# Optimization experiments

Hardware: AMD Instinct MI355X
Metric: run time of the kernel (lower is better)

The kernel has to match this reference:

```python
import jax, jax.numpy as jnp
import numpy as np
import math

D_MODEL = 1024
N_HEADS = 16
B, T = 4, 2048


def setup_inputs() -> dict:
    key = jax.random.key(0)
    ks = jax.random.split(key, 10)
    s = 1.0 / math.sqrt(D_MODEL)
    x = jax.random.normal(ks[0], (B, T, D_MODEL), dtype=jnp.float32)
    # causal mask, broadcastable over batch and heads; 0 -> masked
    mask = jnp.tril(jnp.ones((T, T), dtype=jnp.int32))[None, None, :, :]
    w_q = jax.random.normal(ks[1], (D_MODEL, D_MODEL), dtype=jnp.float32) * s
    b_q = jnp.zeros((D_MODEL,), dtype=jnp.float32)
    w_k = jax.random.normal(ks[2], (D_MODEL, D_MODEL), dtype=jnp.float32) * s
    b_k = jnp.zeros((D_MODEL,), dtype=jnp.float32)
    w_v = jax.random.normal(ks[3], (D_MODEL, D_MODEL), dtype=jnp.float32) * s
    b_v = jnp.zeros((D_MODEL,), dtype=jnp.float32)
    w_o = jax.random.normal(ks[4], (D_MODEL, D_MODEL), dtype=jnp.float32) * s
    b_o = jnp.zeros((D_MODEL,), dtype=jnp.float32)
    return {"x": x, "mask": mask, "w_q": w_q, "b_q": b_q, "w_k": w_k,
            "b_k": b_k, "w_v": w_v, "b_v": b_v, "w_o": w_o, "b_o": b_o}


def reference(x, mask, w_q, b_q, w_k, b_k, w_v, b_v, w_o, b_o):
    Bx, Tx, C = x.shape
    H = N_HEADS
    d_k = C // H
    def split_heads(y):  # [B,T,C] -> [B,H,T,d_k]
        return y.reshape(Bx, Tx, H, d_k).transpose(0, 2, 1, 3)
    Q = split_heads(x @ w_q + b_q)
    K = split_heads(x @ w_k + b_k)
    V = split_heads(x @ w_v + b_v)
    scores = jnp.einsum('bhqd,bhkd->bhqk', Q, K) / math.sqrt(d_k)
    scores = jnp.where(mask == 0, jnp.float32(-1e9), scores)
    attn = jax.nn.softmax(scores, axis=-1)
    out = jnp.einsum('bhqk,bhkd->bhqd', attn, V)
    out = out.transpose(0, 2, 1, 3).reshape(Bx, Tx, C)
    return out @ w_o + b_o
```

## Files before the change

### kernel.cpp

```cpp
#include <hip/hip_runtime.h>
#include <stdint.h>

#define D_MODEL 1024
#define NH      16
#define BB      4
#define TT      2048
#define MROWS   (BB * TT)

typedef __attribute__((ext_vector_type(8))) short bf16x8;
typedef __attribute__((ext_vector_type(4))) float f32x4;

__device__ __forceinline__ unsigned short f2bf(float f) {
    union { float f; unsigned int u; } v; v.f = f;
    unsigned int r = v.u + 0x7fffu + ((v.u >> 16) & 1u);
    return (unsigned short)(r >> 16);
}

__device__ __forceinline__ unsigned short f2bf_fast(float f) {
    union { float f; unsigned int u; } v; v.f = f;
    return (unsigned short)((v.u + 0x8000u) >> 16);
}

__device__ __forceinline__ void gload_lds16(const unsigned short* g, unsigned short* l) {
    __builtin_amdgcn_global_load_lds(
        (const __attribute__((address_space(1))) void*)g,
        (__attribute__((address_space(3))) void*)l,
        16, 0, 0);
}

__global__ void convert_x_kernel(const float* __restrict__ x, unsigned short* __restrict__ xb) {
    int i = blockIdx.x * 256 + threadIdx.x;
    float4 v = ((const float4*)x)[i];
    ushort4 o;
    o.x = f2bf(v.x); o.y = f2bf(v.y); o.z = f2bf(v.z); o.w = f2bf(v.w);
    ((ushort4*)xb)[i] = o;
}

__global__ void transpose_w_kernel(const float* __restrict__ wq, const float* __restrict__ wk,
                                   const float* __restrict__ wv, const float* __restrict__ wo,
                                   unsigned short* tq, unsigned short* tk,
                                   unsigned short* tv, unsigned short* to_) {
    const float* src; unsigned short* dst;
    switch (blockIdx.z) {
        case 0:  src = wq; dst = tq; break;
        case 1:  src = wk; dst = tk; break;
        case 2:  src = wv; dst = tv; break;
        default: src = wo; dst = to_; break;
    }
    __shared__ float tile[32][33];
    int tx = threadIdx.x & 31, ty = threadIdx.x >> 5;
    int k0 = blockIdx.y * 32, n0 = blockIdx.x * 32;
    #pragma unroll
    for (int i = 0; i < 4; ++i)
        tile[ty + i * 8][tx] = src[(k0 + ty + i * 8) * D_MODEL + n0 + tx];
    __syncthreads();
    #pragma unroll
    for (int i = 0; i < 4; ++i)
        dst[(n0 + ty + i * 8) * D_MODEL + k0 + tx] = f2bf(tile[tx][ty + i * 8]);
}

__device__ __forceinline__ void gemm_mainloop(const unsigned short* __restrict__ A,
                                              const unsigned short* __restrict__ Bt,
                                              int m0, int n0,
                                              unsigned short* As, unsigned short* Bs,
                                              f32x4 acc[4][4]) {
    const int tid = threadIdx.x;
    const int lane = tid & 63, wave = tid >> 6;
    const int wm = (wave >> 1) * 64, wn = (wave & 1) * 64;
    const int l15 = lane & 15, quad = lane >> 4;
    const int rx7 = l15 & 7;
    const int srow = tid >> 3;
    const int scol = ((tid & 7) ^ (srow & 7)) * 8;
    const unsigned short* Ag = A + (size_t)(m0 + srow) * D_MODEL + scol;
    const unsigned short* Bg = Bt + (size_t)(n0 + srow) * D_MODEL + scol;
    unsigned short* AsW = As + wave * 512;
    unsigned short* BsW = Bs + wave * 512;
    for (int k0 = 0; k0 < D_MODEL; k0 += 64) {
        __syncthreads();
        #pragma unroll
        for (int p = 0; p < 4; ++p) {
            gload_lds16(Ag + k0 + (size_t)(32 * p) * D_MODEL, AsW + (32 * p) * 64);
            gload_lds16(Bg + k0 + (size_t)(32 * p) * D_MODEL, BsW + (32 * p) * 64);
        }
        __syncthreads();
        #pragma unroll
        for (int kk = 0; kk < 2; ++kk) {
            const int co = ((kk * 4 + quad) ^ rx7) * 8;
            bf16x8 af[4], bfr[4];
            #pragma unroll
            for (int mt = 0; mt < 4; ++mt)
                af[mt] = *(const bf16x8*)(As + (wm + mt * 16 + l15) * 64 + co);
            #pragma unroll
            for (int nt = 0; nt < 4; ++nt)
                bfr[nt] = *(const bf16x8*)(Bs + (wn + nt * 16 + l15) * 64 + co);
            #pragma unroll
            for (int mt = 0; mt < 4; ++mt)
                #pragma unroll
                for (int nt = 0; nt < 4; ++nt)
                    acc[mt][nt] = __builtin_amdgcn_mfma_f32_16x16x32_bf16(af[mt], bfr[nt], acc[mt][nt], 0, 0, 0);
        }
    }
}

__global__ __launch_bounds__(256, 2) void gemm_qkv_kernel(
        const unsigned short* __restrict__ Xb, const unsigned short* __restrict__ Wt,
        const float* __restrict__ bq, const float* __restrict__ bk, const float* __restrict__ bv,
        unsigned short* __restrict__ Qo, unsigned short* __restrict__ Ko,
        unsigned short* __restrict__ VTo) {
    __shared__ unsigned short S[18432];
    unsigned short* As = S;
    unsigned short* Bs = S + 8192;
    int m0 = blockIdx.y * 128, n0 = blockIdx.x * 128;
    f32x4 acc[4][4];
    #pragma unroll
    for (int mt = 0; mt < 4; ++mt)
        #pragma unroll
        for (int nt = 0; nt < 4; ++nt)
            acc[mt][nt] = (f32x4){0.f, 0.f, 0.f, 0.f};
    gemm_mainloop(Xb, Wt, m0, n0, As, Bs, acc);

    const int sel = n0 >> 10;
    const float* bias = (sel == 0) ? bq : (sel == 1) ? bk : bv;
    const float scale = (sel == 0) ? 0.125f * 1.44269504f : 1.f;
    const int tid = threadIdx.x, lane = tid & 63, wave = tid >> 6;
    const int wm = (wave >> 1) * 64, wn = (wave & 1) * 64, l15 = lane & 15, quad = lane >> 4;
    if (sel < 2) {
        unsigned short* Out = (sel == 0) ? Qo : Ko;
        __syncthreads();
        unsigned short* R = S + (wn >> 6) * 9216;
        #pragma unroll
        for (int nt = 0; nt < 4; ++nt) {
            int ln = nt * 16 + l15;
            int col = (n0 + wn + nt * 16 + l15) & 1023;
            float bv_ = bias[col];
            #pragma unroll
            for (int mt = 0; mt < 4; ++mt)
                #pragma unroll
                for (int r = 0; r < 4; ++r) {
                    int lm = wm + mt * 16 + quad * 4 + r;
                    R[lm * 72 + ln] = f2bf((acc[mt][nt][r] + bv_) * scale);
                }
        }
        __syncthreads();
        int hh = tid >> 7, t = tid & 127;
        int h0 = (n0 & 1023) >> 6;
        int b = m0 >> 11, tb = m0 & 2047;
        unsigned short* gp = Out + (size_t)((b * NH + h0 + hh) * TT + tb + t) * 64;
        const unsigned short* lp = S + hh * 9216 + t * 72;
        #pragma unroll
        for (int j = 0; j < 8; ++j)
            *(uint4*)(gp + j * 8) = *(const uint4*)(lp + j * 8);
    } else {
        #pragma unroll
        for (int nt = 0; nt < 4; ++nt) {
            int col = (n0 + wn + nt * 16 + l15) & 1023;
            float bv_ = bias[col];
            int h = col >> 6, dd = col & 63;
            #pragma unroll
            for (int mt = 0; mt < 4; ++mt) {
                int gm0 = m0 + wm + mt * 16 + quad * 4;
                int b = gm0 >> 11, t0 = gm0 & 2047;
                ushort4 o;
                o.x = f2bf(acc[mt][nt][0] + bv_);
                o.y = f2bf(acc[mt][nt][1] + bv_);
                o.z = f2bf(acc[mt][nt][2] + bv_);
                o.w = f2bf(acc[mt][nt][3] + bv_);
                *(ushort4*)&VTo[(((size_t)(b * NH + h) * 16 + (t0 >> 7)) * 64 + dd) * 128 + (t0 & 127)] = o;
            }
        }
    }
}

__global__ __launch_bounds__(256, 2) void gemm_out_kernel(
        const unsigned short* __restrict__ Ob, const unsigned short* __restrict__ Wto,
        const float* __restrict__ bo, float* __restrict__ out) {
    __shared__ unsigned short As[128 * 64], Bs[128 * 64];
    int m0 = blockIdx.y * 128, n0 = blockIdx.x * 128;
    f32x4 acc[4][4];
    #pragma unroll
    for (int mt = 0; mt < 4; ++mt)
        #pragma unroll
        for (int nt = 0; nt < 4; ++nt)
            acc[mt][nt] = (f32x4){0.f, 0.f, 0.f, 0.f};
    gemm_mainloop(Ob, Wto, m0, n0, As, Bs, acc);
    const int tid = threadIdx.x, lane = tid & 63, wave = tid >> 6;
    const int wm = (wave >> 1) * 64, wn = (wave & 1) * 64, l15 = lane & 15, quad = lane >> 4;
    #pragma unroll
    for (int nt = 0; nt < 4; ++nt) {
        int gn = n0 + wn + nt * 16 + l15;
        float bv_ = bo[gn];
        #pragma unroll
        for (int mt = 0; mt < 4; ++mt) {
            #pragma unroll
            for (int r = 0; r < 4; ++r) {
                int gm = m0 + wm + mt * 16 + quad * 4 + r;
                out[(size_t)gm * D_MODEL + gn] = acc[mt][nt][r] + bv_;
            }
        }
    }
}

__global__ __launch_bounds__(256, 3) void flash_kernel(
        const unsigned short* __restrict__ Q, const unsigned short* __restrict__ K,
        const unsigned short* __restrict__ VT, unsigned short* __restrict__ O) {
    __shared__ unsigned short S[21504];
    unsigned short* Kd = S;
    unsigned short* Vd = S + 8192;
    unsigned short* Ps = S + 16384;
    const int n = blockIdx.x;
    const int bh = n & 63;
    const int qt = 15 - (n >> 6);
    const int q0 = qt * 128;
    const int tid = threadIdx.x, lane = tid & 63, wave = tid >> 6;
    const int l15 = lane & 15, quad = lane >> 4;
    const int mbase = wave * 32;
    const unsigned short* Qb = Q + (size_t)bh * (TT * 64) + (size_t)q0 * 64;
    const unsigned short* Kb = K + (size_t)bh * (TT * 64);
    const unsigned short* Vtb = VT + (size_t)bh * (16 * 8192);
    unsigned short* Pw = Ps + wave * 1280;

    int koff[2], voff[2];
    #pragma unroll
    for (int p = 0; p < 2; ++p) {
        int c = p * 256 + tid;
        int r = c >> 3, s = c & 7;
        koff[p] = r * 64 + ((s ^ (r & 7)) * 8);
        voff[p] = r * 128 + ((s ^ (r & 7)) * 8);
    }
    auto fire = [&](int kt, int buf) {
        const unsigned short* Ksrc = Kb + kt * 4096;
        const unsigned short* Vsrc = Vtb + (kt >> 1) * 8192 + (kt & 1) * 64;
        #pragma unroll
        for (int p = 0; p < 2; ++p) {
            gload_lds16(Ksrc + koff[p], Kd + buf * 4096 + (p * 256 + wave * 64) * 8);
            gload_lds16(Vsrc + voff[p], Vd + buf * 4096 + (p * 256 + wave * 64) * 8);
        }
    };

    bf16x8 qf[2][2];
    #pragma unroll
    for (int mt = 0; mt < 2; ++mt)
        #pragma unroll
        for (int kk = 0; kk < 2; ++kk)
            qf[mt][kk] = *(const bf16x8*)(Qb + (size_t)(mbase + mt * 16 + l15) * 64 + kk * 32 + quad * 8);

    float l_part[2][4];
    f32x4 acc[2][4];
    #pragma unroll
    for (int mt = 0; mt < 2; ++mt) {
        #pragma unroll
        for (int r = 0; r < 4; ++r) l_part[mt][r] = 0.f;
        #pragma unroll
        for (int nt = 0; nt < 4; ++nt) acc[mt][nt] = (f32x4){0.f, 0.f, 0.f, 0.f};
    }

    fire(0, 0);

    const int nkt = 2 * qt + 2;
    for (int kt = 0; kt < nkt; ++kt) {
        const int p = kt & 1;
        __syncthreads();
        if (kt + 1 < nkt) fire(kt + 1, p ^ 1);
        if (kt * 64 > q0 + mbase + 31) continue;
        const unsigned short* Ksl = Kd + p * 4096;
        const unsigned short* Vsl = Vd + p * 4096;

        #pragma unroll 1
        for (int s4 = 0; s4 < 2; ++s4) {
            f32x4 sf[2][2];
            #pragma unroll
            for (int mt = 0; mt < 2; ++mt)
                #pragma unroll
                for (int ntl = 0; ntl < 2; ++ntl) sf[mt][ntl] = (f32x4){0.f, 0.f, 0.f, 0.f};
            __builtin_amdgcn_s_setprio(1);
            #pragma unroll
            for (int kk = 0; kk < 2; ++kk)
                #pragma unroll
                for (int ntl = 0; ntl < 2; ++ntl) {
                    int row = s4 * 32 + ntl * 16 + l15;
                    bf16x8 kf = *(const bf16x8*)&Ksl[row * 64 + (((kk * 4 + quad) ^ (row & 7)) * 8)];
                    #pragma unroll
                    for (int mt = 0; mt < 2; ++mt)
                        sf[mt][ntl] = __builtin_amdgcn_mfma_f32_16x16x32_bf16(qf[mt][kk], kf, sf[mt][ntl], 0, 0, 0);
                }
            __builtin_amdgcn_s_setprio(0);
            if (kt >= 2 * qt) {
                const int kofs = (kt - 2 * qt) * 64;
                #pragma unroll
                for (int mt = 0; mt < 2; ++mt)
                    #pragma unroll
                    for (int ntl = 0; ntl < 2; ++ntl)
                        #pragma unroll
                        for (int r = 0; r < 4; ++r) {
                            int qi = mbase + mt * 16 + quad * 4 + r;
                            int ki = kofs + s4 * 32 + ntl * 16 + l15;
                            if (ki > qi) sf[mt][ntl][r] = -1e30f;
                        }
            }
            #pragma unroll
            for (int mt = 0; mt < 2; ++mt)
                #pragma unroll
                for (int ntl = 0; ntl < 2; ++ntl)
                    #pragma unroll
                    for (int r = 0; r < 4; ++r) {
                        float pv = __builtin_amdgcn_exp2f(sf[mt][ntl][r]);
                        l_part[mt][r] += pv;
                        Pw[(mt * 16 + quad * 4 + r) * 40 + ntl * 16 + l15] = f2bf_fast(pv);
                    }
            bf16x8 pa[2];
            #pragma unroll
            for (int mt = 0; mt < 2; ++mt)
                pa[mt] = *(const bf16x8*)&Pw[(mt * 16 + l15) * 40 + quad * 8];
            __builtin_amdgcn_s_setprio(1);
            #pragma unroll
            for (int ntv = 0; ntv < 4; ++ntv) {
                int d = ntv * 16 + l15;
                bf16x8 vf = *(const bf16x8*)&Vsl[d * 64 + (((s4 * 4 + quad) ^ (d & 7)) * 8)];
                #pragma unroll
                for (int mt = 0; mt < 2; ++mt)
                    acc[mt][ntv] = __builtin_amdgcn_mfma_f32_16x16x32_bf16(pa[mt], vf, acc[mt][ntv], 0, 0, 0);
            }
            __builtin_amdgcn_s_setprio(0);
        }
    }

    const int b = bh >> 4, h = bh & 15;
    float inv[2][4];
    #pragma unroll
    for (int mt = 0; mt < 2; ++mt)
        #pragma unroll
        for (int r = 0; r < 4; ++r) {
            float l = l_part[mt][r];
            l += __shfl_xor(l, 1); l += __shfl_xor(l, 2);
            l += __shfl_xor(l, 4); l += __shfl_xor(l, 8);
            inv[mt][r] = __builtin_amdgcn_rcpf(l);
        }
    __syncthreads();
    unsigned short* Ost = S;
    #pragma unroll
    for (int mt = 0; mt < 2; ++mt)
        #pragma unroll
        for (int nt = 0; nt < 4; ++nt)
            #pragma unroll
            for (int r = 0; r < 4; ++r)
                Ost[(mbase + mt * 16 + quad * 4 + r) * 72 + nt * 16 + l15] =
                    f2bf(acc[mt][nt][r] * inv[mt][r]);
    __syncthreads();
    {
        int row = tid >> 1, seg = tid & 1;
        unsigned short* gp = O + (size_t)(b * TT + q0 + row) * D_MODEL + h * 64 + seg * 32;
        const unsigned short* lp = Ost + row * 72 + seg * 32;
        #pragma unroll
        for (int j = 0; j < 4; ++j)
            *(uint4*)(gp + j * 8) = *(const uint4*)(lp + j * 8);
    }
}

extern "C" void kernel_launch(void* const* d_in, const int* in_sizes, int n_in,
                              void* d_out, int out_size, void* d_ws, size_t ws_size,
                              hipStream_t stream) {
    const float* x  = (const float*)d_in[0];
    const float* wq = (const float*)d_in[2];
    const float* bq = (const float*)d_in[3];
    const float* wk = (const float*)d_in[4];
    const float* bk = (const float*)d_in[5];
    const float* wv = (const float*)d_in[6];
    const float* bv = (const float*)d_in[7];
    const float* wo = (const float*)d_in[8];
    const float* bo = (const float*)d_in[9];

    char* ws = (char*)d_ws;
    unsigned short* Xb  = (unsigned short*)ws;
    unsigned short* Wtq = (unsigned short*)(ws + (size_t)(16 << 20));
    unsigned short* Wtk = Wtq + (size_t)D_MODEL * D_MODEL;
    unsigned short* Wtv = Wtk + (size_t)D_MODEL * D_MODEL;
    unsigned short* Wto = Wtv + (size_t)D_MODEL * D_MODEL;
    unsigned short* Qb  = Wto + (size_t)D_MODEL * D_MODEL;
    unsigned short* Kb  = Qb + (size_t)MROWS * D_MODEL;
    unsigned short* VTb = Kb + (size_t)MROWS * D_MODEL;
    unsigned short* Ob  = Xb;

    convert_x_kernel<<<(MROWS * D_MODEL) / (256 * 4), 256, 0, stream>>>(x, Xb);
    transpose_w_kernel<<<dim3(32, 32, 4), 256, 0, stream>>>(wq, wk, wv, wo, Wtq, Wtk, Wtv, Wto);
    gemm_qkv_kernel<<<dim3(3 * D_MODEL / 128, MROWS / 128), 256, 0, stream>>>(
        Xb, Wtq, bq, bk, bv, Qb, Kb, VTb);
    flash_kernel<<<dim3(16 * 64), 256, 0, stream>>>(Qb, Kb, VTb, Ob);
    gemm_out_kernel<<<dim3(D_MODEL / 128, MROWS / 128), 256, 0, stream>>>(Ob, Wto, bo, (float*)d_out);
}
```

Measured before the change: 263.9 us.

## Keep softmax P in registers via transposed QK^T and 16x16x16 MFMA

Swaps the MFMA operands for QK^T so each lane holds scores for one query row across four key columns. That layout matches the A-operand of a 16x16x16 bf16 MFMA, so P is packed straight into registers and the LDS round-trip for P is gone. The PV product now uses 16x16x16 MFMAs with 4-element V loads, and the row-sum reduction is reorganized with cross-quad shuffles. Shared memory shrinks, so launch bounds rise to 4 blocks per CU. The tradeoff is twice as many smaller MFMA instructions and narrower LDS reads for V.

After: 264.4 us. No clear change (+0.2%).

```diff
diff --git a/kernel.cpp b/kernel.cpp
--- a/kernel.cpp
+++ b/kernel.cpp
@@ -8,6 +8,7 @@
 #define MROWS   (BB * TT)
 
 typedef __attribute__((ext_vector_type(8))) short bf16x8;
+typedef __attribute__((ext_vector_type(4))) short bf16x4;
 typedef __attribute__((ext_vector_type(4))) float f32x4;
 
 __device__ __forceinline__ unsigned short f2bf(float f) {
@@ -19,6 +20,11 @@
 __device__ __forceinline__ unsigned short f2bf_fast(float f) {
     union { float f; unsigned int u; } v; v.f = f;
     return (unsigned short)((v.u + 0x8000u) >> 16);
+}
+
+__device__ __forceinline__ f32x4 mfma_16x16x16_bf16(bf16x4 a, bf16x4 b, f32x4 c) {
+    asm("v_mfma_f32_16x16x16_bf16 %0, %1, %2, %0" : "+v"(c) : "v"(a), "v"(b));
+    return c;
 }
 
 __device__ __forceinline__ void gload_lds16(const unsigned short* g, unsigned short* l) {
@@ -200,13 +206,12 @@
     }
 }
 
-__global__ __launch_bounds__(256, 3) void flash_kernel(
+__global__ __launch_bounds__(256, 4) void flash_kernel(
         const unsigned short* __restrict__ Q, const unsigned short* __restrict__ K,
         const unsigned short* __restrict__ VT, unsigned short* __restrict__ O) {
-    __shared__ unsigned short S[21504];
+    __shared__ unsigned short S[16384];
     unsigned short* Kd = S;
     unsigned short* Vd = S + 8192;
-    unsigned short* Ps = S + 16384;
     const int n = blockIdx.x;
     const int bh = n & 63;
     const int qt = 15 - (n >> 6);
@@ -217,7 +222,6 @@
     const unsigned short* Qb = Q + (size_t)bh * (TT * 64) + (size_t)q0 * 64;
     const unsigned short* Kb = K + (size_t)bh * (TT * 64);
     const unsigned short* Vtb = VT + (size_t)bh * (16 * 8192);
-    unsigned short* Pw = Ps + wave * 1280;
 
     int koff[2], voff[2];
     #pragma unroll
@@ -244,15 +248,12 @@
         for (int kk = 0; kk < 2; ++kk)
             qf[mt][kk] = *(const bf16x8*)(Qb + (size_t)(mbase + mt * 16 + l15) * 64 + kk * 32 + quad * 8);
 
-    float l_part[2][4];
+    float l_full[2] = {0.f, 0.f};
     f32x4 acc[2][4];
     #pragma unroll
-    for (int mt = 0; mt < 2; ++mt) {
-        #pragma unroll
-        for (int r = 0; r < 4; ++r) l_part[mt][r] = 0.f;
+    for (int mt = 0; mt < 2; ++mt)
         #pragma unroll
         for (int nt = 0; nt < 4; ++nt) acc[mt][nt] = (f32x4){0.f, 0.f, 0.f, 0.f};
-    }
 
     fire(0, 0);
 
@@ -281,44 +282,52 @@
                     bf16x8 kf = *(const bf16x8*)&Ksl[row * 64 + (((kk * 4 + quad) ^ (row & 7)) * 8)];
                     #pragma unroll
                     for (int mt = 0; mt < 2; ++mt)
-                        sf[mt][ntl] = __builtin_amdgcn_mfma_f32_16x16x32_bf16(qf[mt][kk], kf, sf[mt][ntl], 0, 0, 0);
+                        sf[mt][ntl] = __builtin_amdgcn_mfma_f32_16x16x32_bf16(kf, qf[mt][kk], sf[mt][ntl], 0, 0, 0);
                 }
             __builtin_amdgcn_s_setprio(0);
             if (kt >= 2 * qt) {
                 const int kofs = (kt - 2 * qt) * 64;
                 #pragma unroll
-                for (int mt = 0; mt < 2; ++mt)
+                for (int mt = 0; mt < 2; ++mt) {
+                    int qi = mbase + mt * 16 + l15;
                     #pragma unroll
                     for (int ntl = 0; ntl < 2; ++ntl)
                         #pragma unroll
                         for (int r = 0; r < 4; ++r) {
-                            int qi = mbase + mt * 16 + quad * 4 + r;
-                            int ki = kofs + s4 * 32 + ntl * 16 + l15;
+                            int ki = kofs + s4 * 32 + ntl * 16 + quad * 4 + r;
                             if (ki > qi) sf[mt][ntl][r] = -1e30f;
                         }
+                }
             }
+            bf16x4 pa[2][2];
             #pragma unroll
             for (int mt = 0; mt < 2; ++mt)
                 #pragma unroll
-                for (int ntl = 0; ntl < 2; ++ntl)
+                for (int ntl = 0; ntl < 2; ++ntl) {
+                    float p0 = __builtin_amdgcn_exp2f(sf[mt][ntl][0]);
+                    float p1 = __builtin_amdgcn_exp2f(sf[mt][ntl][1]);
+                    float p2 = __builtin_amdgcn_exp2f(sf[mt][ntl][2]);
+                    float p3 = __builtin_amdgcn_exp2f(sf[mt][ntl][3]);
+                    l_full[mt] += (p0 + p1) + (p2 + p3);
+                    bf16x4 pk;
+                    pk[0] = (short)f2bf_fast(p0);
+                    pk[1] = (short)f2bf_fast(p1);
+                    pk[2] = (short)f2bf_fast(p2);
+                    pk[3] = (short)f2bf_fast(p3);
+                    pa[mt][ntl] = pk;
+                }
+            __builtin_amdgcn_s_setprio(1);
+            #pragma unroll
+            for (int ntl = 0; ntl < 2; ++ntl) {
+                #pragma unroll
+                for (int ntv = 0; ntv < 4; ++ntv) {
+                    int d = ntv * 16 + l15;
+                    int cch = s4 * 4 + ntl * 2 + (quad >> 1);
+                    bf16x4 vf = *(const bf16x4*)&Vsl[d * 64 + ((cch ^ (d & 7)) * 8) + (quad & 1) * 4];
                     #pragma unroll
-                    for (int r = 0; r < 4; ++r) {
-                        float pv = __builtin_amdgcn_exp2f(sf[mt][ntl][r]);
-                        l_part[mt][r] += pv;
-                        Pw[(mt * 16 + quad * 4 + r) * 40 + ntl * 16 + l15] = f2bf_fast(pv);
-                    }
-            bf16x8 pa[2];
-            #pragma unroll
-            for (int mt = 0; mt < 2; ++mt)
-                pa[mt] = *(const bf16x8*)&Pw[(mt * 16 + l15) * 40 + quad * 8];
-            __builtin_amdgcn_s_setprio(1);
-            #pragma unroll
-            for (int ntv = 0; ntv < 4; ++ntv) {
-                int d = ntv * 16 + l15;
-                bf16x8 vf = *(const bf16x8*)&Vsl[d * 64 + (((s4 * 4 + quad) ^ (d & 7)) * 8)];
-                #pragma unroll
-                for (int mt = 0; mt < 2; ++mt)
-                    acc[mt][ntv] = __builtin_amdgcn_mfma_f32_16x16x32_bf16(pa[mt], vf, acc[mt][ntv], 0, 0, 0);
+                    for (int mt = 0; mt < 2; ++mt)
+                        acc[mt][ntv] = mfma_16x16x16_bf16(pa[mt][ntl], vf, acc[mt][ntv]);
+                }
             }
             __builtin_amdgcn_s_setprio(0);
         }
@@ -327,14 +336,16 @@
     const int b = bh >> 4, h = bh & 15;
     float inv[2][4];
     #pragma unroll
-    for (int mt = 0; mt < 2; ++mt)
+    for (int mt = 0; mt < 2; ++mt) {
+        float l = l_full[mt];
+        l += __shfl_xor(l, 16);
+        l += __shfl_xor(l, 32);
         #pragma unroll
         for (int r = 0; r < 4; ++r) {
-            float l = l_part[mt][r];
-            l += __shfl_xor(l, 1); l += __shfl_xor(l, 2);
-            l += __shfl_xor(l, 4); l += __shfl_xor(l, 8);
-            inv[mt][r] = __builtin_amdgcn_rcpf(l);
-        }
+            float lr = __shfl(l, quad * 4 + r);
+            inv[mt][r] = __builtin_amdgcn_rcpf(lr);
+        }
+    }
     __syncthreads();
     unsigned short* Ost = S;
     #pragma unroll
```
